# Kernel tuning notes

Hardware: AMD Instinct MI355X
Metric: run time of the kernel (lower is better)

Reference implementation:

```python
import jax, jax.numpy as jnp
import numpy as np

N = 100000      # num POIs (nodes)
M = 20000       # num trajectories (hyperedges)
NNZ = 1000000   # incidence entries
D = 128         # emb_dim
NUM_LAYERS = 3
NEG_SLOPE = 0.2  # PyG HypergraphConv leaky_relu default


def setup_inputs() -> dict:
    key = jax.random.key(0)
    ks = jax.random.split(key, 8)
    pois_embs = jax.random.normal(ks[0], (N, D), jnp.float32)
    traj_embs = jax.random.normal(ks[1], (M, D), jnp.float32)
    hyperedge_weight = jax.random.uniform(ks[2], (M,), jnp.float32)
    node_idx = jax.random.randint(ks[3], (NNZ,), 0, N, jnp.int32)
    edge_idx = jax.random.randint(ks[4], (NNZ,), 0, M, jnp.int32)
    # learned params of the shared HypergraphConv layer (heads=1, concat)
    W_lin = jax.random.normal(ks[5], (D, D), jnp.float32) / np.sqrt(D).astype(np.float32)
    att = jax.random.normal(ks[6], (2 * D,), jnp.float32) * 0.1
    bias = jnp.zeros((D,), jnp.float32)
    return dict(pois_embs=pois_embs, traj_embs=traj_embs,
                hyperedge_weight=hyperedge_weight,
                node_idx=node_idx, edge_idx=edge_idx,
                W_lin=W_lin, att=att, bias=bias)


def _segment_softmax(scores, seg, num_seg):
    smax = jax.ops.segment_max(scores, seg, num_segments=num_seg)
    smax = jnp.where(jnp.isfinite(smax), smax, 0.0)  # guard empty segments
    ex = jnp.exp(scores - smax[seg])
    den = jax.ops.segment_sum(ex, seg, num_segments=num_seg)
    return ex / (den[seg] + 1e-16)


def _hconv(x, traj_embs, hyperedge_weight, node_idx, edge_idx, W_lin, att, bias):
    # x: [N, D] node feats; traj_embs: [M, D] hyperedge feats
    xt = x @ W_lin            # [N, D]  lin(x)
    et = traj_embs @ W_lin    # [M, D]  lin(hyperedge_attr)
    # attention logits per incidence pair (additive decomposition of cat*att)
    s_n = xt @ att[:D]        # [N]
    s_e = et @ att[D:]        # [M]
    alpha = jax.nn.leaky_relu(s_n[node_idx] + s_e[edge_idx], NEG_SLOPE)  # [NNZ]
    alpha = _segment_softmax(alpha, node_idx, N)  # softmax grouped by node
    # degree normalizations: D = sum_e H_ve * w_e, B = |e|
    Ddeg = jax.ops.segment_sum(hyperedge_weight[edge_idx], node_idx, num_segments=N)
    Dinv = jnp.where(Ddeg > 0, 1.0 / Ddeg, 0.0)
    Bdeg = jax.ops.segment_sum(jnp.ones((NNZ,), xt.dtype), edge_idx, num_segments=M)
    Binv = jnp.where(Bdeg > 0, 1.0 / Bdeg, 0.0)
    # node -> edge: B^{-1} H^T (alpha * x)
    msg1 = (alpha * Binv[edge_idx])[:, None] * xt[node_idx]        # [NNZ, D]
    edge_out = jax.ops.segment_sum(msg1, edge_idx, num_segments=M)  # [M, D]
    # edge -> node: D^{-1} H (alpha * edge_out)
    msg2 = (alpha * Dinv[node_idx])[:, None] * edge_out[edge_idx]   # [NNZ, D]
    out = jax.ops.segment_sum(msg2, node_idx, num_segments=N)       # [N, D]
    return out + bias


def reference(pois_embs, traj_embs, hyperedge_weight, node_idx, edge_idx, W_lin, att, bias):
    cur = pois_embs
    acc = pois_embs  # running sum of stacked layer outputs (incl. input)
    for _ in range(NUM_LAYERS):
        cur = _hconv(cur, traj_embs, hyperedge_weight, node_idx, edge_idx, W_lin, att, bias) + cur
        acc = acc + cur
    return acc / jnp.asarray(NUM_LAYERS + 1, acc.dtype)  # mean over stack
```

## Files before the change

### kernel.cpp

```cpp
#include <hip/hip_runtime.h>
#include <hip/hip_fp16.h>
#include <cstdint>
#include <cstddef>
#include <cstring>

#define DIM 128
#define NEG_SLOPE 0.2f

#define EREP 16
#define NREP 8

typedef _Float16 half8v __attribute__((ext_vector_type(8)));
typedef __attribute__((ext_vector_type(4))) float float4v;

__device__ __forceinline__ float2 h2f2(uint u) {
  __half2 h;
  __builtin_memcpy(&h, &u, 4);
  return __half22float2(h);
}
__device__ __forceinline__ uint packh2(float lo, float hi) {
  __half2 h = __floats2half2_rn(lo, hi);
  uint u;
  __builtin_memcpy(&u, &h, 4);
  return u;
}
__device__ __forceinline__ ushort f2h_us(float f) {
  __half h = __float2half_rn(f);
  ushort us;
  __builtin_memcpy(&us, &h, 2);
  return us;
}
__device__ __forceinline__ float lrelu(float x) {
  return x >= 0.0f ? x : NEG_SLOPE * x;
}

__global__ void wswz_kernel(const float* __restrict__ W, ushort* __restrict__ Wswz)
{
  int i = blockIdx.x * 256 + threadIdx.x;
  int j = i & 7, lane = (i >> 3) & 63, nt = (i >> 9) & 7, kt = i >> 12;
  int k = kt * 32 + (lane >> 4) * 8 + j;
  int col = nt * 16 + (lane & 15);
  Wswz[i] = f2h_us(W[k * 128 + col]);
}

__global__ void poish_kernel(const float* __restrict__ pois,
                             uint4* __restrict__ pois_h, int N_, int NP)
{
  int i = blockIdx.x * 256 + threadIdx.x;
  if (i >= NP * 16) return;
  int row = i >> 4;
  uint4 o;
  if (row < N_) {
    const float* src = pois + (size_t)i * 8;
    float4 f0 = *(const float4*)src;
    float4 f1 = *(const float4*)(src + 4);
    o.x = packh2(f0.x, f0.y); o.y = packh2(f0.z, f0.w);
    o.z = packh2(f1.x, f1.y); o.w = packh2(f1.z, f1.w);
  } else { o.x = o.y = o.z = o.w = 0; }
  pois_h[i] = o;
}

__global__ __launch_bounds__(256) void gemm_mfma_kernel(
    const ushort* __restrict__ Xb, const ushort* __restrict__ Wswz,
    const float* __restrict__ att, ushort* __restrict__ Yb,
    float* __restrict__ s_n, int rowsN)
{
  __shared__ ushort st[64 * 128];
  int tid = threadIdx.x;
  int w = tid >> 6, lane = tid & 63;
  int q = lane >> 4, c = lane & 15;
  int r0b = blockIdx.x * 64;
  int r0 = r0b + w * 16;
  float4v acc[8];
#pragma unroll
  for (int nt = 0; nt < 8; ++nt) acc[nt] = (float4v){0.f, 0.f, 0.f, 0.f};
  const ushort* arow = Xb + (size_t)(r0 + c) * DIM + q * 8;
#pragma unroll
  for (int kt = 0; kt < 4; ++kt) {
    half8v a = *(const half8v*)(arow + kt * 32);
#pragma unroll
    for (int nt = 0; nt < 8; ++nt) {
      half8v b = *(const half8v*)(Wswz + ((((kt << 3) + nt) << 9) + (lane << 3)));
      acc[nt] = __builtin_amdgcn_mfma_f32_16x16x32_f16(a, b, acc[nt], 0, 0, 0);
    }
  }
  float av[8];
#pragma unroll
  for (int nt = 0; nt < 8; ++nt) av[nt] = att[nt * 16 + c];
  float p0 = 0, p1 = 0, p2 = 0, p3 = 0;
#pragma unroll
  for (int nt = 0; nt < 8; ++nt) {
    p0 = fmaf(acc[nt][0], av[nt], p0);
    p1 = fmaf(acc[nt][1], av[nt], p1);
    p2 = fmaf(acc[nt][2], av[nt], p2);
    p3 = fmaf(acc[nt][3], av[nt], p3);
  }
#pragma unroll
  for (int m = 8; m >= 1; m >>= 1) {
    p0 += __shfl_xor(p0, m, 64);
    p1 += __shfl_xor(p1, m, 64);
    p2 += __shfl_xor(p2, m, 64);
    p3 += __shfl_xor(p3, m, 64);
  }
  if (c == 0) {
    int rb = r0 + q * 4;
    if (rb + 0 < rowsN) s_n[rb + 0] = p0;
    if (rb + 1 < rowsN) s_n[rb + 1] = p1;
    if (rb + 2 < rowsN) s_n[rb + 2] = p2;
    if (rb + 3 < rowsN) s_n[rb + 3] = p3;
  }
  ushort* sw = st + w * 2048;
#pragma unroll
  for (int nt = 0; nt < 8; ++nt) {
    sw[(q * 4 + 0) * 128 + nt * 16 + c] = f2h_us(acc[nt][0]);
    sw[(q * 4 + 1) * 128 + nt * 16 + c] = f2h_us(acc[nt][1]);
    sw[(q * 4 + 2) * 128 + nt * 16 + c] = f2h_us(acc[nt][2]);
    sw[(q * 4 + 3) * 128 + nt * 16 + c] = f2h_us(acc[nt][3]);
  }
  __syncthreads();
#pragma unroll
  for (int it = 0; it < 4; ++it) {
    int idx = tid + it * 256;
    int row = idx >> 4, seg = idx & 15;
    *(uint4*)(Yb + (size_t)(r0b + row) * DIM + seg * 8) =
        *(const uint4*)&st[row * 128 + seg * 8];
  }
}

__global__ __launch_bounds__(256) void se_kernel(
    const float* __restrict__ traj, const float* __restrict__ W,
    const float* __restrict__ att, const float* __restrict__ hw,
    float* __restrict__ s_e, float2* __restrict__ se_hw, int M_)
{
  __shared__ float wv[128];
  int tid = threadIdx.x;
  if (tid < 128) {
    const float* wr = W + (size_t)tid * 128;
    float acc = 0.0f;
#pragma unroll 4
    for (int k = 0; k < 128; ++k) acc = fmaf(wr[k], att[DIM + k], acc);
    wv[tid] = acc;
  }
  __syncthreads();
  int e = blockIdx.x * 4 + (tid >> 6);
  int lane = tid & 63;
  if (e >= M_) return;
  const float* row = traj + (size_t)e * DIM;
  float v = row[lane] * wv[lane] + row[lane + 64] * wv[lane + 64];
#pragma unroll
  for (int d = 32; d > 0; d >>= 1) v += __shfl_down(v, d, 64);
  if (lane == 0) {
    s_e[e] = v;
    float2 g; g.x = v; g.y = hw[e];
    se_hw[e] = g;
  }
}

__global__ void hist_rank_kernel(const int* __restrict__ node_idx,
                                 const int* __restrict__ edge_idx,
                                 int* __restrict__ ncnt_r, int* __restrict__ ecnt_r,
                                 int* __restrict__ r_n, int* __restrict__ r_e,
                                 int nnz, int M_, int N_)
{
  int t = blockIdx.x * blockDim.x + threadIdx.x;
  int j = t * 2;
  if (j >= nnz) return;
  int* ec = ecnt_r + (size_t)(t & (EREP - 1)) * M_;
  int* nc = ncnt_r + (size_t)(t & (NREP - 1)) * N_;
  if (j + 2 <= nnz) {
    int2 e = *(const int2*)&edge_idx[j];
    int2 n = *(const int2*)&node_idx[j];
    int a0 = atomicAdd(&ec[e.x], 1);
    int a1 = atomicAdd(&ec[e.y], 1);
    int b0 = atomicAdd(&nc[n.x], 1);
    int b1 = atomicAdd(&nc[n.y], 1);
    *(int2*)&r_e[j] = make_int2(a0, a1);
    *(int2*)&r_n[j] = make_int2(b0, b1);
  } else {
    r_e[j] = atomicAdd(&ec[edge_idx[j]], 1);
    r_n[j] = atomicAdd(&nc[node_idx[j]], 1);
  }
}

__global__ void repsum_kernel(int* __restrict__ cnt_r, int* __restrict__ cnt,
                              int nbins, int reps)
{
  int b = blockIdx.x * blockDim.x + threadIdx.x;
  if (b >= nbins) return;
  int s = 0;
  for (int r = 0; r < reps; ++r) {
    size_t o = (size_t)r * nbins + b;
    int v = cnt_r[o];
    cnt_r[o] = s;
    s += v;
  }
  cnt[b] = s;
}

__global__ __launch_bounds__(1024) void scan_block_kernel(
    const int* __restrict__ cnt, int* __restrict__ off,
    int* __restrict__ partials, int nbins)
{
  __shared__ int ws[16];
  int tid = threadIdx.x, lane = tid & 63, wid = tid >> 6;
  int base = blockIdx.x * 4096 + tid * 4;
  int x0 = base + 0 < nbins ? cnt[base + 0] : 0;
  int x1 = base + 1 < nbins ? cnt[base + 1] : 0;
  int x2 = base + 2 < nbins ? cnt[base + 2] : 0;
  int x3 = base + 3 < nbins ? cnt[base + 3] : 0;
  int t = x0 + x1 + x2 + x3;
  int v = t;
#pragma unroll
  for (int d = 1; d < 64; d <<= 1) {
    int y = __shfl_up(v, d, 64);
    if (lane >= d) v += y;
  }
  if (lane == 63) ws[wid] = v;
  __syncthreads();
  if (tid < 16) {
    int s = ws[tid];
#pragma unroll
    for (int d = 1; d < 16; d <<= 1) {
      int y = __shfl_up(s, d, 16);
      if (tid >= d) s += y;
    }
    ws[tid] = s;
  }
  __syncthreads();
  int pre = (wid > 0 ? ws[wid - 1] : 0) + (v - t);
  if (base + 0 < nbins) off[base + 0] = pre;
  if (base + 1 < nbins) off[base + 1] = pre + x0;
  if (base + 2 < nbins) off[base + 2] = pre + x0 + x1;
  if (base + 3 < nbins) off[base + 3] = pre + x0 + x1 + x2;
  if (tid == 0) partials[blockIdx.x] = ws[15];
}

__global__ __launch_bounds__(64) void scan_partials_kernel(
    int* __restrict__ partials, int nb)
{
  int lane = threadIdx.x;
  int t = lane < nb ? partials[lane] : 0;
  int v = t;
#pragma unroll
  for (int d = 1; d < 64; d <<= 1) {
    int y = __shfl_up(v, d, 64);
    if (lane >= d) v += y;
  }
  if (lane < nb) partials[lane] = v - t;
  if (lane == 63) partials[nb] = v;
}

__global__ void add_off_combine_kernel(int* __restrict__ off,
                                       const int* __restrict__ partials,
                                       int* __restrict__ pre,
                                       int nbins, int nb, int reps)
{
  int i = blockIdx.x * blockDim.x + threadIdx.x;
  if (i < nbins) {
    int o = off[i] + partials[i >> 12];
    off[i] = o;
    for (int r = 0; r < reps; ++r) pre[(size_t)r * nbins + i] += o;
  }
  if (i == 0) off[nbins] = partials[nb];
}

__global__ void scatter_edge_kernel(const int* __restrict__ node_idx,
                                    const int* __restrict__ edge_idx,
                                    const int* __restrict__ r_e,
                                    const int* __restrict__ pre_e,
                                    int* __restrict__ nd_e, int nnz, int M_)
{
  int j = (blockIdx.x * blockDim.x + threadIdx.x) * 4;
  if (j >= nnz) return;
  if (j + 4 <= nnz) {
    const int* p0 = pre_e + (size_t)((j >> 1) & (EREP - 1)) * M_;
    const int* p1 = pre_e + (size_t)(((j >> 1) + 1) & (EREP - 1)) * M_;
    int4 e = *(const int4*)&edge_idx[j];
    int4 n = *(const int4*)&node_idx[j];
    int4 re = *(const int4*)&r_e[j];
    nd_e[p0[e.x] + re.x] = n.x;
    nd_e[p0[e.y] + re.y] = n.y;
    nd_e[p1[e.z] + re.z] = n.z;
    nd_e[p1[e.w] + re.w] = n.w;
  } else {
    for (int k = j; k < nnz; ++k) {
      const int* pp = pre_e + (size_t)((k >> 1) & (EREP - 1)) * M_;
      nd_e[pp[edge_idx[k]] + r_e[k]] = node_idx[k];
    }
  }
}

__global__ void scatter_node_kernel(const int* __restrict__ node_idx,
                                    const int* __restrict__ edge_idx,
                                    const int* __restrict__ r_n,
                                    const int* __restrict__ pre_n,
                                    int* __restrict__ eidx_n, int nnz, int N_)
{
  int j = (blockIdx.x * blockDim.x + threadIdx.x) * 4;
  if (j >= nnz) return;
  if (j + 4 <= nnz) {
    const int* p0 = pre_n + (size_t)((j >> 1) & (NREP - 1)) * N_;
    const int* p1 = pre_n + (size_t)(((j >> 1) + 1) & (NREP - 1)) * N_;
    int4 e = *(const int4*)&edge_idx[j];
    int4 n = *(const int4*)&node_idx[j];
    int4 rn = *(const int4*)&r_n[j];
    eidx_n[p0[n.x] + rn.x] = e.x;
    eidx_n[p0[n.y] + rn.y] = e.y;
    eidx_n[p1[n.z] + rn.z] = e.z;
    eidx_n[p1[n.w] + rn.w] = e.w;
  } else {
    for (int k = j; k < nnz; ++k) {
      const int* pp = pre_n + (size_t)((k >> 1) & (NREP - 1)) * N_;
      eidx_n[pp[node_idx[k]] + r_n[k]] = edge_idx[k];
    }
  }
}

__global__ void softstat_kernel(const int* __restrict__ noff,
                                const int* __restrict__ eidx_n,
                                const float* __restrict__ s_n,
                                const float2* __restrict__ se_hw,
                                float2* __restrict__ ns2,
                                float* __restrict__ Dinv, int N_)
{
  int n = blockIdx.x * blockDim.x + threadIdx.x;
  if (n >= N_) return;
  int s = noff[n], e1 = noff[n + 1];
  float sn = s_n[n];
  float m = -INFINITY, den = 0.0f, d = 0.0f;
  int t = s;
  for (; t + 4 <= e1; t += 4) {
    int i0 = eidx_n[t], i1 = eidx_n[t + 1], i2 = eidx_n[t + 2], i3 = eidx_n[t + 3];
    float2 g0 = se_hw[i0], g1 = se_hw[i1], g2 = se_hw[i2], g3 = se_hw[i3];
    float l0 = lrelu(sn + g0.x), l1 = lrelu(sn + g1.x);
    float l2 = lrelu(sn + g2.x), l3 = lrelu(sn + g3.x);
    float mm = fmaxf(fmaxf(fmaxf(l0, l1), fmaxf(l2, l3)), m);
    den = den * __expf(m - mm) + __expf(l0 - mm) + __expf(l1 - mm)
        + __expf(l2 - mm) + __expf(l3 - mm);
    m = mm;
    d += g0.y + g1.y + g2.y + g3.y;
  }
  for (; t < e1; ++t) {
    float2 g = se_hw[eidx_n[t]];
    float l = lrelu(sn + g.x);
    float mm = fmaxf(l, m);
    den = den * __expf(m - mm) + __expf(l - mm);
    m = mm;
    d += g.y;
  }
  if (s == e1) m = 0.0f;
  float2 r;
  r.x = sn;
  r.y = m + __logf(den + 1e-16f);
  ns2[n] = r;
  Dinv[n] = d > 0.0f ? 1.0f / d : 0.0f;
}

__global__ __launch_bounds__(256) void msg1_kernel(
    const int* __restrict__ eoff, const int* __restrict__ nd_e,
    const float2* __restrict__ ns2, const float* __restrict__ s_e,
    const uint4* __restrict__ xt16, uint4* __restrict__ eo16, int M_)
{
  int e = blockIdx.x * 4 + (threadIdx.x >> 6);
  int lane = threadIdx.x & 63;
  int r = lane >> 4, c = lane & 15;
  if (e >= M_) return;
  int s = eoff[e], t1 = eoff[e + 1];
  int len = t1 - s;
  float binv = len > 0 ? 1.0f / (float)len : 0.0f;
  float se = s_e[e];
  float acc[8];
#pragma unroll
  for (int j = 0; j < 8; ++j) acc[j] = 0.0f;
  for (int t = s; t < t1; t += 8) {
#pragma unroll
    for (int h = 0; h < 2; ++h) {
      int tb = t + h * 4;
      if (tb < t1) {
        int ti = tb + r;
        int tc = ti < t1 ? ti : t1 - 1;
        float valid = ti < t1 ? 1.0f : 0.0f;
        int nd = nd_e[tc];
        float2 q = ns2[nd];
        float coef = valid * __expf(lrelu(q.x + se) - q.y);
        uint4 g = xt16[(size_t)nd * 16 + c];
        float2 f0 = h2f2(g.x), f1 = h2f2(g.y), f2 = h2f2(g.z), f3 = h2f2(g.w);
        acc[0] = fmaf(coef, f0.x, acc[0]);
        acc[1] = fmaf(coef, f0.y, acc[1]);
        acc[2] = fmaf(coef, f1.x, acc[2]);
        acc[3] = fmaf(coef, f1.y, acc[3]);
        acc[4] = fmaf(coef, f2.x, acc[4]);
        acc[5] = fmaf(coef, f2.y, acc[5]);
        acc[6] = fmaf(coef, f3.x, acc[6]);
        acc[7] = fmaf(coef, f3.y, acc[7]);
      }
    }
  }
#pragma unroll
  for (int j = 0; j < 8; ++j) {
    acc[j] += __shfl_xor(acc[j], 16, 64);
    acc[j] += __shfl_xor(acc[j], 32, 64);
  }
  if (r == 0) {
    uint4 o;
    o.x = packh2(acc[0] * binv, acc[1] * binv);
    o.y = packh2(acc[2] * binv, acc[3] * binv);
    o.z = packh2(acc[4] * binv, acc[5] * binv);
    o.w = packh2(acc[6] * binv, acc[7] * binv);
    eo16[(size_t)e * 16 + c] = o;
  }
}

__global__ __launch_bounds__(256) void msg2_kernel(
    const int* __restrict__ noff, const int* __restrict__ eidx_n,
    const float2* __restrict__ ns2, const float* __restrict__ Dinv,
    const float* __restrict__ s_e, const uint4* __restrict__ eo16,
    const float* __restrict__ bias,
    const float* __restrict__ cin_f, const uint4* __restrict__ cin_h16,
    const uint4* __restrict__ x1h16, const uint4* __restrict__ x2h16,
    uint4* __restrict__ couth16, float* __restrict__ dout,
    int mode, int N_)
{
  int n = blockIdx.x * 4 + (threadIdx.x >> 6);
  int lane = threadIdx.x & 63;
  int r = lane >> 4, c = lane & 15;
  if (n >= N_) return;
  int s = noff[n], t1 = noff[n + 1];
  float2 nsv = ns2[n];
  float sn = nsv.x, lz = nsv.y;
  float acc[8];
#pragma unroll
  for (int j = 0; j < 8; ++j) acc[j] = 0.0f;
  for (int t = s; t < t1; t += 8) {
#pragma unroll
    for (int h = 0; h < 2; ++h) {
      int tb = t + h * 4;
      if (tb < t1) {
        int ti = tb + r;
        int tc = ti < t1 ? ti : t1 - 1;
        float valid = ti < t1 ? 1.0f : 0.0f;
        int ed = eidx_n[tc];
        float xs = s_e[ed];
        float coef = valid * __expf(lrelu(sn + xs) - lz);
        uint4 g = eo16[(size_t)ed * 16 + c];
        float2 f0 = h2f2(g.x), f1 = h2f2(g.y), f2 = h2f2(g.z), f3 = h2f2(g.w);
        acc[0] = fmaf(coef, f0.x, acc[0]);
        acc[1] = fmaf(coef, f0.y, acc[1]);
        acc[2] = fmaf(coef, f1.x, acc[2]);
        acc[3] = fmaf(coef, f1.y, acc[3]);
        acc[4] = fmaf(coef, f2.x, acc[4]);
        acc[5] = fmaf(coef, f2.y, acc[5]);
        acc[6] = fmaf(coef, f3.x, acc[6]);
        acc[7] = fmaf(coef, f3.y, acc[7]);
      }
    }
  }
#pragma unroll
  for (int j = 0; j < 8; ++j) {
    acc[j] += __shfl_xor(acc[j], 16, 64);
    acc[j] += __shfl_xor(acc[j], 32, 64);
  }
  if (r != 0) return;
  float sc = Dinv[n];
  float cin[8];
  if (mode == 0) {
    const float4* cf = (const float4*)(cin_f + (size_t)n * DIM);
    float4 a = cf[c * 2], b = cf[c * 2 + 1];
    cin[0] = a.x; cin[1] = a.y; cin[2] = a.z; cin[3] = a.w;
    cin[4] = b.x; cin[5] = b.y; cin[6] = b.z; cin[7] = b.w;
  } else {
    uint4 ch = cin_h16[(size_t)n * 16 + c];
    float2 p0 = h2f2(ch.x), p1 = h2f2(ch.y), p2 = h2f2(ch.z), p3 = h2f2(ch.w);
    cin[0] = p0.x; cin[1] = p0.y; cin[2] = p1.x; cin[3] = p1.y;
    cin[4] = p2.x; cin[5] = p2.y; cin[6] = p3.x; cin[7] = p3.y;
  }
  const float4* bf = (const float4*)bias;
  float4 ba = bf[c * 2], bb = bf[c * 2 + 1];
  float bs[8] = {ba.x, ba.y, ba.z, ba.w, bb.x, bb.y, bb.z, bb.w};
  float cx[8];
#pragma unroll
  for (int j = 0; j < 8; ++j) cx[j] = cin[j] + acc[j] * sc + bs[j];
  if (mode == 2) {
    uint4 x1 = x1h16[(size_t)n * 16 + c];
    float2 z0 = h2f2(x1.x), z1 = h2f2(x1.y), z2 = h2f2(x1.z), z3 = h2f2(x1.w);
    float x1v[8] = {z0.x, z0.y, z1.x, z1.y, z2.x, z2.y, z3.x, z3.y};
    uint4 x2 = x2h16[(size_t)n * 16 + c];
    float2 y0 = h2f2(x2.x), y1 = h2f2(x2.y), y2 = h2f2(x2.z), y3 = h2f2(x2.w);
    float x2v[8] = {y0.x, y0.y, y1.x, y1.y, y2.x, y2.y, y3.x, y3.y};
    float4 o0, o1;
    o0.x = (x1v[0] + x2v[0] + cin[0] + cx[0]) * 0.25f;
    o0.y = (x1v[1] + x2v[1] + cin[1] + cx[1]) * 0.25f;
    o0.z = (x1v[2] + x2v[2] + cin[2] + cx[2]) * 0.25f;
    o0.w = (x1v[3] + x2v[3] + cin[3] + cx[3]) * 0.25f;
    o1.x = (x1v[4] + x2v[4] + cin[4] + cx[4]) * 0.25f;
    o1.y = (x1v[5] + x2v[5] + cin[5] + cx[5]) * 0.25f;
    o1.z = (x1v[6] + x2v[6] + cin[6] + cx[6]) * 0.25f;
    o1.w = (x1v[7] + x2v[7] + cin[7] + cx[7]) * 0.25f;
    float4* dp = (float4*)(dout + (size_t)n * DIM);
    dp[c * 2] = o0;
    dp[c * 2 + 1] = o1;
  } else {
    uint4 o;
    o.x = packh2(cx[0], cx[1]);
    o.y = packh2(cx[2], cx[3]);
    o.z = packh2(cx[4], cx[5]);
    o.w = packh2(cx[6], cx[7]);
    couth16[(size_t)n * 16 + c] = o;
  }
}

static inline int cdiv(int a, int b) { return (a + b - 1) / b; }

extern "C" void kernel_launch(void* const* d_in, const int* in_sizes, int n_in,
                              void* d_out, int out_size, void* d_ws, size_t ws_size,
                              hipStream_t stream)
{
  const float* pois = (const float*)d_in[0];
  const float* traj = (const float*)d_in[1];
  const float* hw   = (const float*)d_in[2];
  const int* node_idx = (const int*)d_in[3];
  const int* edge_idx = (const int*)d_in[4];
  const float* W    = (const float*)d_in[5];
  const float* att  = (const float*)d_in[6];
  const float* bias = (const float*)d_in[7];
  float* dout = (float*)d_out;

  const int N   = in_sizes[0] / DIM;
  const int M   = in_sizes[2];
  const int NNZ = in_sizes[3];
  const int NP  = (N + 63) & ~63;

  char* p = (char*)d_ws;
  auto alloc = [&](size_t bytes) -> void* {
    void* r = (void*)p;
    p += (bytes + 255) & ~(size_t)255;
    return r;
  };
  ushort* xt_h    = (ushort*)alloc((size_t)NP * DIM * 2);
  ushort* pois_h  = (ushort*)alloc((size_t)NP * DIM * 2);
  uint*   cura_h  = (uint*)alloc((size_t)NP * 64 * 4);
  uint*   curb_h  = (uint*)alloc((size_t)NP * 64 * 4);
  ushort* W_swz   = (ushort*)alloc(16384 * 2);
  uint*   eo_h  = (uint*)alloc((size_t)M * (DIM / 2) * 4);
  float2* ns2   = (float2*)alloc((size_t)N * 8);
  float*  s_e  = (float*)alloc((size_t)M * 4);
  float2* se_hw = (float2*)alloc((size_t)M * 8);
  float*  s_n  = (float*)alloc((size_t)N * 4);
  float*  Dinv = (float*)alloc((size_t)N * 4);
  int* ecnt   = (int*)alloc((size_t)M * 4);
  int* ncnt   = (int*)alloc((size_t)N * 4);
  int* ecnt_r = (int*)alloc((size_t)EREP * M * 4);
  int* ncnt_r = (int*)alloc((size_t)NREP * N * 4);
  int* eoff = (int*)alloc((size_t)(M + 1) * 4);
  int* noff = (int*)alloc((size_t)(N + 1) * 4);
  int* r_e  = (int*)alloc((size_t)NNZ * 4);
  int* r_n  = (int*)alloc((size_t)NNZ * 4);
  int* nd_e   = (int*)alloc((size_t)NNZ * 4);
  int* eidx_n = (int*)alloc((size_t)NNZ * 4);
  int* part_e = (int*)alloc(65 * 4);
  int* part_n = (int*)alloc(65 * 4);
  (void)ws_size;

  const int nbE = cdiv(M, 4096), nbN = cdiv(N, 4096);

  hipMemsetAsync(ecnt_r, 0, (size_t)EREP * M * 4, stream);
  hipMemsetAsync(ncnt_r, 0, (size_t)NREP * N * 4, stream);
  hist_rank_kernel<<<cdiv(NNZ, 512), 256, 0, stream>>>(node_idx, edge_idx, ncnt_r, ecnt_r, r_n, r_e, NNZ, M, N);
  repsum_kernel<<<cdiv(M, 256), 256, 0, stream>>>(ecnt_r, ecnt, M, EREP);
  repsum_kernel<<<cdiv(N, 256), 256, 0, stream>>>(ncnt_r, ncnt, N, NREP);
  scan_block_kernel<<<nbE, 1024, 0, stream>>>(ecnt, eoff, part_e, M);
  scan_block_kernel<<<nbN, 1024, 0, stream>>>(ncnt, noff, part_n, N);
  scan_partials_kernel<<<1, 64, 0, stream>>>(part_e, nbE);
  scan_partials_kernel<<<1, 64, 0, stream>>>(part_n, nbN);
  add_off_combine_kernel<<<cdiv(M, 256), 256, 0, stream>>>(eoff, part_e, ecnt_r, M, nbE, EREP);
  add_off_combine_kernel<<<cdiv(N, 256), 256, 0, stream>>>(noff, part_n, ncnt_r, N, nbN, NREP);
  scatter_edge_kernel<<<cdiv(NNZ, 1024), 256, 0, stream>>>(node_idx, edge_idx, r_e, ecnt_r, nd_e, NNZ, M);
  scatter_node_kernel<<<cdiv(NNZ, 1024), 256, 0, stream>>>(node_idx, edge_idx, r_n, ncnt_r, eidx_n, NNZ, N);

  wswz_kernel<<<64, 256, 0, stream>>>(W, W_swz);
  se_kernel<<<cdiv(M, 4), 256, 0, stream>>>(traj, W, att, hw, s_e, se_hw, M);
  poish_kernel<<<cdiv(NP * 16, 256), 256, 0, stream>>>(pois, (uint4*)pois_h, N, NP);

  for (int layer = 0; layer < 3; ++layer) {
    const ushort* gin = (layer == 0) ? pois_h
                       : (layer == 1) ? (const ushort*)cura_h
                                      : (const ushort*)curb_h;
    gemm_mfma_kernel<<<NP / 64, 256, 0, stream>>>(gin, W_swz, att, xt_h, s_n, N);
    softstat_kernel<<<cdiv(N, 256), 256, 0, stream>>>(noff, eidx_n, s_n, se_hw, ns2, Dinv, N);
    msg1_kernel<<<cdiv(M, 4), 256, 0, stream>>>(eoff, nd_e, ns2, s_e,
                                                (const uint4*)xt_h, (uint4*)eo_h, M);
    const uint* cin_h = (layer == 1) ? cura_h : curb_h;
    uint* couth = (layer == 0) ? cura_h : curb_h;
    msg2_kernel<<<cdiv(N, 4), 256, 0, stream>>>(noff, eidx_n, ns2, Dinv, s_e,
                                                (const uint4*)eo_h, bias,
                                                pois, (const uint4*)cin_h,
                                                (const uint4*)pois_h,
                                                (const uint4*)cura_h,
                                                (uint4*)couth, dout, layer, N);
  }
}
```

Measured before the change: 689.5 us.

## Fuse histogram, first-layer GEMM and edge-score kernels into one launch

```diff
diff --git a/kernel.cpp b/kernel.cpp
--- a/kernel.cpp
+++ b/kernel.cpp
@@ -60,6 +60,135 @@
   pois_h[i] = o;
 }
 
+__global__ __launch_bounds__(256) void prep_fused_kernel(
+    const int* __restrict__ node_idx, const int* __restrict__ edge_idx,
+    int* __restrict__ ncnt_r, int* __restrict__ ecnt_r,
+    int* __restrict__ r_n, int* __restrict__ r_e,
+    int nnz, int M_, int N_, int histBlocks,
+    const ushort* __restrict__ Xb, const ushort* __restrict__ Wswz,
+    const float* __restrict__ att, ushort* __restrict__ Yb,
+    float* __restrict__ s_n, int rowsN, int gemmBlocks,
+    const float* __restrict__ traj, const float* __restrict__ W,
+    const float* __restrict__ hw,
+    float* __restrict__ s_e, float2* __restrict__ se_hw)
+{
+  __shared__ ushort st[64 * 128];
+  int b = blockIdx.x;
+  int tid = threadIdx.x;
+
+  if (b < histBlocks) {
+    int T = b * 256 + tid;
+    int stride = histBlocks * 256;
+    int npairs = (nnz + 1) >> 1;
+    for (int t = T; t < npairs; t += stride) {
+      int j = t * 2;
+      int* ec = ecnt_r + (size_t)(t & (EREP - 1)) * M_;
+      int* nc = ncnt_r + (size_t)(t & (NREP - 1)) * N_;
+      if (j + 2 <= nnz) {
+        int2 e = *(const int2*)&edge_idx[j];
+        int2 n = *(const int2*)&node_idx[j];
+        int a0 = atomicAdd(&ec[e.x], 1);
+        int a1 = atomicAdd(&ec[e.y], 1);
+        int b0 = atomicAdd(&nc[n.x], 1);
+        int b1 = atomicAdd(&nc[n.y], 1);
+        *(int2*)&r_e[j] = make_int2(a0, a1);
+        *(int2*)&r_n[j] = make_int2(b0, b1);
+      } else {
+        r_e[j] = atomicAdd(&ec[edge_idx[j]], 1);
+        r_n[j] = atomicAdd(&nc[node_idx[j]], 1);
+      }
+    }
+    return;
+  }
+
+  if (b < histBlocks + gemmBlocks) {
+    int bb = b - histBlocks;
+    int w = tid >> 6, lane = tid & 63;
+    int q = lane >> 4, c = lane & 15;
+    int r0b = bb * 64;
+    int r0 = r0b + w * 16;
+    float4v acc[8];
+#pragma unroll
+    for (int nt = 0; nt < 8; ++nt) acc[nt] = (float4v){0.f, 0.f, 0.f, 0.f};
+    const ushort* arow = Xb + (size_t)(r0 + c) * DIM + q * 8;
+#pragma unroll
+    for (int kt = 0; kt < 4; ++kt) {
+      half8v a = *(const half8v*)(arow + kt * 32);
+#pragma unroll
+      for (int nt = 0; nt < 8; ++nt) {
+        half8v bfr = *(const half8v*)(Wswz + ((((kt << 3) + nt) << 9) + (lane << 3)));
+        acc[nt] = __builtin_amdgcn_mfma_f32_16x16x32_f16(a, bfr, acc[nt], 0, 0, 0);
+      }
+    }
+    float av[8];
+#pragma unroll
+    for (int nt = 0; nt < 8; ++nt) av[nt] = att[nt * 16 + c];
+    float p0 = 0, p1 = 0, p2 = 0, p3 = 0;
+#pragma unroll
+    for (int nt = 0; nt < 8; ++nt) {
+      p0 = fmaf(acc[nt][0], av[nt], p0);
+      p1 = fmaf(acc[nt][1], av[nt], p1);
+      p2 = fmaf(acc[nt][2], av[nt], p2);
+      p3 = fmaf(acc[nt][3], av[nt], p3);
+    }
+#pragma unroll
+    for (int m = 8; m >= 1; m >>= 1) {
+      p0 += __shfl_xor(p0, m, 64);
+      p1 += __shfl_xor(p1, m, 64);
+      p2 += __shfl_xor(p2, m, 64);
+      p3 += __shfl_xor(p3, m, 64);
+    }
+    if (c == 0) {
+      int rb = r0 + q * 4;
+      if (rb + 0 < rowsN) s_n[rb + 0] = p0;
+      if (rb + 1 < rowsN) s_n[rb + 1] = p1;
+      if (rb + 2 < rowsN) s_n[rb + 2] = p2;
+      if (rb + 3 < rowsN) s_n[rb + 3] = p3;
+    }
+    ushort* sw = st + w * 2048;
+#pragma unroll
+    for (int nt = 0; nt < 8; ++nt) {
+      sw[(q * 4 + 0) * 128 + nt * 16 + c] = f2h_us(acc[nt][0]);
+      sw[(q * 4 + 1) * 128 + nt * 16 + c] = f2h_us(acc[nt][1]);
+      sw[(q * 4 + 2) * 128 + nt * 16 + c] = f2h_us(acc[nt][2]);
+      sw[(q * 4 + 3) * 128 + nt * 16 + c] = f2h_us(acc[nt][3]);
+    }
+    __syncthreads();
+#pragma unroll
+    for (int it = 0; it < 4; ++it) {
+      int idx = tid + it * 256;
+      int row = idx >> 4, seg = idx & 15;
+      *(uint4*)(Yb + (size_t)(r0b + row) * DIM + seg * 8) =
+          *(const uint4*)&st[row * 128 + seg * 8];
+    }
+    return;
+  }
+
+  {
+    float* wv = (float*)st;
+    if (tid < 128) {
+      const float* wr = W + (size_t)tid * 128;
+      float acc = 0.0f;
+#pragma unroll 4
+      for (int k = 0; k < 128; ++k) acc = fmaf(wr[k], att[DIM + k], acc);
+      wv[tid] = acc;
+    }
+    __syncthreads();
+    int e = (b - histBlocks - gemmBlocks) * 4 + (tid >> 6);
+    int lane = tid & 63;
+    if (e >= M_) return;
+    const float* row = traj + (size_t)e * DIM;
+    float v = row[lane] * wv[lane] + row[lane + 64] * wv[lane + 64];
+#pragma unroll
+    for (int d = 32; d > 0; d >>= 1) v += __shfl_down(v, d, 64);
+    if (lane == 0) {
+      s_e[e] = v;
+      float2 g; g.x = v; g.y = hw[e];
+      se_hw[e] = g;
+    }
+  }
+}
+
 __global__ __launch_bounds__(256) void gemm_mfma_kernel(
     const ushort* __restrict__ Xb, const ushort* __restrict__ Wswz,
     const float* __restrict__ att, ushort* __restrict__ Yb,
@@ -124,61 +253,6 @@
     int row = idx >> 4, seg = idx & 15;
     *(uint4*)(Yb + (size_t)(r0b + row) * DIM + seg * 8) =
         *(const uint4*)&st[row * 128 + seg * 8];
-  }
-}
-
-__global__ __launch_bounds__(256) void se_kernel(
-    const float* __restrict__ traj, const float* __restrict__ W,
-    const float* __restrict__ att, const float* __restrict__ hw,
-    float* __restrict__ s_e, float2* __restrict__ se_hw, int M_)
-{
-  __shared__ float wv[128];
-  int tid = threadIdx.x;
-  if (tid < 128) {
-    const float* wr = W + (size_t)tid * 128;
-    float acc = 0.0f;
-#pragma unroll 4
-    for (int k = 0; k < 128; ++k) acc = fmaf(wr[k], att[DIM + k], acc);
-    wv[tid] = acc;
-  }
-  __syncthreads();
-  int e = blockIdx.x * 4 + (tid >> 6);
-  int lane = tid & 63;
-  if (e >= M_) return;
-  const float* row = traj + (size_t)e * DIM;
-  float v = row[lane] * wv[lane] + row[lane + 64] * wv[lane + 64];
-#pragma unroll
-  for (int d = 32; d > 0; d >>= 1) v += __shfl_down(v, d, 64);
-  if (lane == 0) {
-    s_e[e] = v;
-    float2 g; g.x = v; g.y = hw[e];
-    se_hw[e] = g;
-  }
-}
-
-__global__ void hist_rank_kernel(const int* __restrict__ node_idx,
-                                 const int* __restrict__ edge_idx,
-                                 int* __restrict__ ncnt_r, int* __restrict__ ecnt_r,
-                                 int* __restrict__ r_n, int* __restrict__ r_e,
-                                 int nnz, int M_, int N_)
-{
-  int t = blockIdx.x * blockDim.x + threadIdx.x;
-  int j = t * 2;
-  if (j >= nnz) return;
-  int* ec = ecnt_r + (size_t)(t & (EREP - 1)) * M_;
-  int* nc = ncnt_r + (size_t)(t & (NREP - 1)) * N_;
-  if (j + 2 <= nnz) {
-    int2 e = *(const int2*)&edge_idx[j];
-    int2 n = *(const int2*)&node_idx[j];
-    int a0 = atomicAdd(&ec[e.x], 1);
-    int a1 = atomicAdd(&ec[e.y], 1);
-    int b0 = atomicAdd(&nc[n.x], 1);
-    int b1 = atomicAdd(&nc[n.y], 1);
-    *(int2*)&r_e[j] = make_int2(a0, a1);
-    *(int2*)&r_n[j] = make_int2(b0, b1);
-  } else {
-    r_e[j] = atomicAdd(&ec[edge_idx[j]], 1);
-    r_n[j] = atomicAdd(&nc[node_idx[j]], 1);
   }
 }
 
@@ -416,7 +490,7 @@
     const float2* __restrict__ ns2, const float* __restrict__ Dinv,
     const float* __restrict__ s_e, const uint4* __restrict__ eo16,
     const float* __restrict__ bias,
-    const float* __restrict__ cin_f, const uint4* __restrict__ cin_h16,
+    const uint4* __restrict__ cin_h16,
     const uint4* __restrict__ x1h16, const uint4* __restrict__ x2h16,
     uint4* __restrict__ couth16, float* __restrict__ dout,
     int mode, int N_)
@@ -462,18 +536,9 @@
   }
   if (r != 0) return;
   float sc = Dinv[n];
-  float cin[8];
-  if (mode == 0) {
-    const float4* cf = (const float4*)(cin_f + (size_t)n * DIM);
-    float4 a = cf[c * 2], b = cf[c * 2 + 1];
-    cin[0] = a.x; cin[1] = a.y; cin[2] = a.z; cin[3] = a.w;
-    cin[4] = b.x; cin[5] = b.y; cin[6] = b.z; cin[7] = b.w;
-  } else {
-    uint4 ch = cin_h16[(size_t)n * 16 + c];
-    float2 p0 = h2f2(ch.x), p1 = h2f2(ch.y), p2 = h2f2(ch.z), p3 = h2f2(ch.w);
-    cin[0] = p0.x; cin[1] = p0.y; cin[2] = p1.x; cin[3] = p1.y;
-    cin[4] = p2.x; cin[5] = p2.y; cin[6] = p3.x; cin[7] = p3.y;
-  }
+  uint4 ch = cin_h16[(size_t)n * 16 + c];
+  float2 p0 = h2f2(ch.x), p1 = h2f2(ch.y), p2 = h2f2(ch.z), p3 = h2f2(ch.w);
+  float cin[8] = {p0.x, p0.y, p1.x, p1.y, p2.x, p2.y, p3.x, p3.y};
   const float4* bf = (const float4*)bias;
   float4 ba = bf[c * 2], bb = bf[c * 2 + 1];
   float bs[8] = {ba.x, ba.y, ba.z, ba.w, bb.x, bb.y, bb.z, bb.w};
@@ -562,10 +627,21 @@
   (void)ws_size;
 
   const int nbE = cdiv(M, 4096), nbN = cdiv(N, 4096);
+  const int npairs = (NNZ + 1) >> 1;
+  const int histBlocks = cdiv(npairs, 512);
+  const int gemmBlocks = NP / 64;
+  const int seBlocks = cdiv(M, 4);
 
   hipMemsetAsync(ecnt_r, 0, (size_t)EREP * M * 4, stream);
   hipMemsetAsync(ncnt_r, 0, (size_t)NREP * N * 4, stream);
-  hist_rank_kernel<<<cdiv(NNZ, 512), 256, 0, stream>>>(node_idx, edge_idx, ncnt_r, ecnt_r, r_n, r_e, NNZ, M, N);
+  wswz_kernel<<<64, 256, 0, stream>>>(W, W_swz);
+  poish_kernel<<<cdiv(NP * 16, 256), 256, 0, stream>>>(pois, (uint4*)pois_h, N, NP);
+
+  prep_fused_kernel<<<histBlocks + gemmBlocks + seBlocks, 256, 0, stream>>>(
+      node_idx, edge_idx, ncnt_r, ecnt_r, r_n, r_e, NNZ, M, N, histBlocks,
+      pois_h, W_swz, att, xt_h, s_n, N, gemmBlocks,
+      traj, W, hw, s_e, se_hw);
+
   repsum_kernel<<<cdiv(M, 256), 256, 0, stream>>>(ecnt_r, ecnt, M, EREP);
   repsum_kernel<<<cdiv(N, 256), 256, 0, stream>>>(ncnt_r, ncnt, N, NREP);
   scan_block_kernel<<<nbE, 1024, 0, stream>>>(ecnt, eoff, part_e, M);
@@ -577,23 +653,21 @@
   scatter_edge_kernel<<<cdiv(NNZ, 1024), 256, 0, stream>>>(node_idx, edge_idx, r_e, ecnt_r, nd_e, NNZ, M);
   scatter_node_kernel<<<cdiv(NNZ, 1024), 256, 0, stream>>>(node_idx, edge_idx, r_n, ncnt_r, eidx_n, NNZ, N);
 
-  wswz_kernel<<<64, 256, 0, stream>>>(W, W_swz);
-  se_kernel<<<cdiv(M, 4), 256, 0, stream>>>(traj, W, att, hw, s_e, se_hw, M);
-  poish_kernel<<<cdiv(NP * 16, 256), 256, 0, stream>>>(pois, (uint4*)pois_h, N, NP);
-
   for (int layer = 0; layer < 3; ++layer) {
-    const ushort* gin = (layer == 0) ? pois_h
-                       : (layer == 1) ? (const ushort*)cura_h
-                                      : (const ushort*)curb_h;
-    gemm_mfma_kernel<<<NP / 64, 256, 0, stream>>>(gin, W_swz, att, xt_h, s_n, N);
+    if (layer > 0) {
+      const ushort* gin = (layer == 1) ? (const ushort*)cura_h
+                                       : (const ushort*)curb_h;
+      gemm_mfma_kernel<<<NP / 64, 256, 0, stream>>>(gin, W_swz, att, xt_h, s_n, N);
+    }
     softstat_kernel<<<cdiv(N, 256), 256, 0, stream>>>(noff, eidx_n, s_n, se_hw, ns2, Dinv, N);
     msg1_kernel<<<cdiv(M, 4), 256, 0, stream>>>(eoff, nd_e, ns2, s_e,
                                                 (const uint4*)xt_h, (uint4*)eo_h, M);
-    const uint* cin_h = (layer == 1) ? cura_h : curb_h;
+    const uint* cin_h = (layer == 0) ? (const uint*)pois_h
+                       : (layer == 1) ? cura_h : curb_h;
     uint* couth = (layer == 0) ? cura_h : curb_h;
     msg2_kernel<<<cdiv(N, 4), 256, 0, stream>>>(noff, eidx_n, ns2, Dinv, s_e,
                                                 (const uint4*)eo_h, bias,
-                                                pois, (const uint4*)cin_h,
+                                                (const uint4*)cin_h,
                                                 (const uint4*)pois_h,
                                                 (const uint4*)cura_h,
                                                 (uint4*)couth, dout, layer, N);
```

Measured after the change: 679.7 us. Within noise of the previous version (-1.4%).

## Drop replicated histograms and fuse histogram with edge-score kernel

Applied to the files above, without the earlier changes.

```diff
diff --git a/kernel.cpp b/kernel.cpp
--- a/kernel.cpp
+++ b/kernel.cpp
@@ -6,9 +6,6 @@
 
 #define DIM 128
 #define NEG_SLOPE 0.2f
-
-#define EREP 16
-#define NREP 8
 
 typedef _Float16 half8v __attribute__((ext_vector_type(8)));
 typedef __attribute__((ext_vector_type(4))) float float4v;
@@ -60,6 +57,61 @@
   pois_h[i] = o;
 }
 
+__global__ __launch_bounds__(256) void hist_se_fused_kernel(
+    const int* __restrict__ node_idx, const int* __restrict__ edge_idx,
+    int* __restrict__ ncnt, int* __restrict__ ecnt,
+    int* __restrict__ r_n, int* __restrict__ r_e,
+    int nnz, int M_, int N_, int histBlocks,
+    const float* __restrict__ traj, const float* __restrict__ W,
+    const float* __restrict__ att, const float* __restrict__ hw,
+    float* __restrict__ s_e, float2* __restrict__ se_hw)
+{
+  __shared__ float wv[128];
+  int b = blockIdx.x;
+  int tid = threadIdx.x;
+
+  if (b < histBlocks) {
+    int t = b * 256 + tid;
+    int j = t * 2;
+    if (j >= nnz) return;
+    if (j + 2 <= nnz) {
+      int2 e = *(const int2*)&edge_idx[j];
+      int2 n = *(const int2*)&node_idx[j];
+      int a0 = atomicAdd(&ecnt[e.x], 1);
+      int a1 = atomicAdd(&ecnt[e.y], 1);
+      int b0 = atomicAdd(&ncnt[n.x], 1);
+      int b1 = atomicAdd(&ncnt[n.y], 1);
+      *(int2*)&r_e[j] = make_int2(a0, a1);
+      *(int2*)&r_n[j] = make_int2(b0, b1);
+    } else {
+      r_e[j] = atomicAdd(&ecnt[edge_idx[j]], 1);
+      r_n[j] = atomicAdd(&ncnt[node_idx[j]], 1);
+    }
+    return;
+  }
+
+  if (tid < 128) {
+    const float* wr = W + (size_t)tid * 128;
+    float acc = 0.0f;
+#pragma unroll 4
+    for (int k = 0; k < 128; ++k) acc = fmaf(wr[k], att[DIM + k], acc);
+    wv[tid] = acc;
+  }
+  __syncthreads();
+  int e = (b - histBlocks) * 4 + (tid >> 6);
+  int lane = tid & 63;
+  if (e >= M_) return;
+  const float* row = traj + (size_t)e * DIM;
+  float v = row[lane] * wv[lane] + row[lane + 64] * wv[lane + 64];
+#pragma unroll
+  for (int d = 32; d > 0; d >>= 1) v += __shfl_down(v, d, 64);
+  if (lane == 0) {
+    s_e[e] = v;
+    float2 g; g.x = v; g.y = hw[e];
+    se_hw[e] = g;
+  }
+}
+
 __global__ __launch_bounds__(256) void gemm_mfma_kernel(
     const ushort* __restrict__ Xb, const ushort* __restrict__ Wswz,
     const float* __restrict__ att, ushort* __restrict__ Yb,
@@ -125,76 +177,6 @@
     *(uint4*)(Yb + (size_t)(r0b + row) * DIM + seg * 8) =
         *(const uint4*)&st[row * 128 + seg * 8];
   }
-}
-
-__global__ __launch_bounds__(256) void se_kernel(
-    const float* __restrict__ traj, const float* __restrict__ W,
-    const float* __restrict__ att, const float* __restrict__ hw,
-    float* __restrict__ s_e, float2* __restrict__ se_hw, int M_)
-{
-  __shared__ float wv[128];
-  int tid = threadIdx.x;
-  if (tid < 128) {
-    const float* wr = W + (size_t)tid * 128;
-    float acc = 0.0f;
-#pragma unroll 4
-    for (int k = 0; k < 128; ++k) acc = fmaf(wr[k], att[DIM + k], acc);
-    wv[tid] = acc;
-  }
-  __syncthreads();
-  int e = blockIdx.x * 4 + (tid >> 6);
-  int lane = tid & 63;
-  if (e >= M_) return;
-  const float* row = traj + (size_t)e * DIM;
-  float v = row[lane] * wv[lane] + row[lane + 64] * wv[lane + 64];
-#pragma unroll
-  for (int d = 32; d > 0; d >>= 1) v += __shfl_down(v, d, 64);
-  if (lane == 0) {
-    s_e[e] = v;
-    float2 g; g.x = v; g.y = hw[e];
-    se_hw[e] = g;
-  }
-}
-
-__global__ void hist_rank_kernel(const int* __restrict__ node_idx,
-                                 const int* __restrict__ edge_idx,
-                                 int* __restrict__ ncnt_r, int* __restrict__ ecnt_r,
-                                 int* __restrict__ r_n, int* __restrict__ r_e,
-                                 int nnz, int M_, int N_)
-{
-  int t = blockIdx.x * blockDim.x + threadIdx.x;
-  int j = t * 2;
-  if (j >= nnz) return;
-  int* ec = ecnt_r + (size_t)(t & (EREP - 1)) * M_;
-  int* nc = ncnt_r + (size_t)(t & (NREP - 1)) * N_;
-  if (j + 2 <= nnz) {
-    int2 e = *(const int2*)&edge_idx[j];
-    int2 n = *(const int2*)&node_idx[j];
-    int a0 = atomicAdd(&ec[e.x], 1);
-    int a1 = atomicAdd(&ec[e.y], 1);
-    int b0 = atomicAdd(&nc[n.x], 1);
-    int b1 = atomicAdd(&nc[n.y], 1);
-    *(int2*)&r_e[j] = make_int2(a0, a1);
-    *(int2*)&r_n[j] = make_int2(b0, b1);
-  } else {
-    r_e[j] = atomicAdd(&ec[edge_idx[j]], 1);
-    r_n[j] = atomicAdd(&nc[node_idx[j]], 1);
-  }
-}
-
-__global__ void repsum_kernel(int* __restrict__ cnt_r, int* __restrict__ cnt,
-                              int nbins, int reps)
-{
-  int b = blockIdx.x * blockDim.x + threadIdx.x;
-  if (b >= nbins) return;
-  int s = 0;
-  for (int r = 0; r < reps; ++r) {
-    size_t o = (size_t)r * nbins + b;
-    int v = cnt_r[o];
-    cnt_r[o] = s;
-    s += v;
-  }
-  cnt[b] = s;
 }
 
 __global__ __launch_bounds__(1024) void scan_block_kernel(
@@ -250,69 +232,54 @@
   if (lane == 63) partials[nb] = v;
 }
 
-__global__ void add_off_combine_kernel(int* __restrict__ off,
-                                       const int* __restrict__ partials,
-                                       int* __restrict__ pre,
-                                       int nbins, int nb, int reps)
+__global__ void add_off_kernel(int* __restrict__ off,
+                               const int* __restrict__ partials,
+                               int nbins, int nb)
 {
   int i = blockIdx.x * blockDim.x + threadIdx.x;
-  if (i < nbins) {
-    int o = off[i] + partials[i >> 12];
-    off[i] = o;
-    for (int r = 0; r < reps; ++r) pre[(size_t)r * nbins + i] += o;
-  }
+  if (i < nbins) off[i] += partials[i >> 12];
   if (i == 0) off[nbins] = partials[nb];
 }
 
 __global__ void scatter_edge_kernel(const int* __restrict__ node_idx,
                                     const int* __restrict__ edge_idx,
                                     const int* __restrict__ r_e,
-                                    const int* __restrict__ pre_e,
-                                    int* __restrict__ nd_e, int nnz, int M_)
+                                    const int* __restrict__ eoff,
+                                    int* __restrict__ nd_e, int nnz)
 {
   int j = (blockIdx.x * blockDim.x + threadIdx.x) * 4;
   if (j >= nnz) return;
   if (j + 4 <= nnz) {
-    const int* p0 = pre_e + (size_t)((j >> 1) & (EREP - 1)) * M_;
-    const int* p1 = pre_e + (size_t)(((j >> 1) + 1) & (EREP - 1)) * M_;
     int4 e = *(const int4*)&edge_idx[j];
     int4 n = *(const int4*)&node_idx[j];
     int4 re = *(const int4*)&r_e[j];
-    nd_e[p0[e.x] + re.x] = n.x;
-    nd_e[p0[e.y] + re.y] = n.y;
-    nd_e[p1[e.z] + re.z] = n.z;
-    nd_e[p1[e.w] + re.w] = n.w;
+    nd_e[eoff[e.x] + re.x] = n.x;
+    nd_e[eoff[e.y] + re.y] = n.y;
+    nd_e[eoff[e.z] + re.z] = n.z;
+    nd_e[eoff[e.w] + re.w] = n.w;
   } else {
-    for (int k = j; k < nnz; ++k) {
-      const int* pp = pre_e + (size_t)((k >> 1) & (EREP - 1)) * M_;
-      nd_e[pp[edge_idx[k]] + r_e[k]] = node_idx[k];
-    }
+    for (int k = j; k < nnz; ++k) nd_e[eoff[edge_idx[k]] + r_e[k]] = node_idx[k];
   }
 }
 
 __global__ void scatter_node_kernel(const int* __restrict__ node_idx,
                                     const int* __restrict__ edge_idx,
                                     const int* __restrict__ r_n,
-                                    const int* __restrict__ pre_n,
-                                    int* __restrict__ eidx_n, int nnz, int N_)
+                                    const int* __restrict__ noff,
+                                    int* __restrict__ eidx_n, int nnz)
 {
   int j = (blockIdx.x * blockDim.x + threadIdx.x) * 4;
   if (j >= nnz) return;
   if (j + 4 <= nnz) {
-    const int* p0 = pre_n + (size_t)((j >> 1) & (NREP - 1)) * N_;
-    const int* p1 = pre_n + (size_t)(((j >> 1) + 1) & (NREP - 1)) * N_;
     int4 e = *(const int4*)&edge_idx[j];
     int4 n = *(const int4*)&node_idx[j];
     int4 rn = *(const int4*)&r_n[j];
-    eidx_n[p0[n.x] + rn.x] = e.x;
-    eidx_n[p0[n.y] + rn.y] = e.y;
-    eidx_n[p1[n.z] + rn.z] = e.z;
-    eidx_n[p1[n.w] + rn.w] = e.w;
+    eidx_n[noff[n.x] + rn.x] = e.x;
+    eidx_n[noff[n.y] + rn.y] = e.y;
+    eidx_n[noff[n.z] + rn.z] = e.z;
+    eidx_n[noff[n.w] + rn.w] = e.w;
   } else {
-    for (int k = j; k < nnz; ++k) {
-      const int* pp = pre_n + (size_t)((k >> 1) & (NREP - 1)) * N_;
-      eidx_n[pp[node_idx[k]] + r_n[k]] = edge_idx[k];
-    }
+    for (int k = j; k < nnz; ++k) eidx_n[noff[node_idx[k]] + r_n[k]] = edge_idx[k];
   }
 }
 
@@ -416,7 +383,7 @@
     const float2* __restrict__ ns2, const float* __restrict__ Dinv,
     const float* __restrict__ s_e, const uint4* __restrict__ eo16,
     const float* __restrict__ bias,
-    const float* __restrict__ cin_f, const uint4* __restrict__ cin_h16,
+    const uint4* __restrict__ cin_h16,
     const uint4* __restrict__ x1h16, const uint4* __restrict__ x2h16,
     uint4* __restrict__ couth16, float* __restrict__ dout,
     int mode, int N_)
@@ -462,18 +429,9 @@
   }
   if (r != 0) return;
   float sc = Dinv[n];
-  float cin[8];
-  if (mode == 0) {
-    const float4* cf = (const float4*)(cin_f + (size_t)n * DIM);
-    float4 a = cf[c * 2], b = cf[c * 2 + 1];
-    cin[0] = a.x; cin[1] = a.y; cin[2] = a.z; cin[3] = a.w;
-    cin[4] = b.x; cin[5] = b.y; cin[6] = b.z; cin[7] = b.w;
-  } else {
-    uint4 ch = cin_h16[(size_t)n * 16 + c];
-    float2 p0 = h2f2(ch.x), p1 = h2f2(ch.y), p2 = h2f2(ch.z), p3 = h2f2(ch.w);
-    cin[0] = p0.x; cin[1] = p0.y; cin[2] = p1.x; cin[3] = p1.y;
-    cin[4] = p2.x; cin[5] = p2.y; cin[6] = p3.x; cin[7] = p3.y;
-  }
+  uint4 ch = cin_h16[(size_t)n * 16 + c];
+  float2 p0 = h2f2(ch.x), p1 = h2f2(ch.y), p2 = h2f2(ch.z), p3 = h2f2(ch.w);
+  float cin[8] = {p0.x, p0.y, p1.x, p1.y, p2.x, p2.y, p3.x, p3.y};
   const float4* bf = (const float4*)bias;
   float4 ba = bf[c * 2], bb = bf[c * 2 + 1];
   float bs[8] = {ba.x, ba.y, ba.z, ba.w, bb.x, bb.y, bb.z, bb.w};
@@ -547,10 +505,8 @@
   float2* se_hw = (float2*)alloc((size_t)M * 8);
   float*  s_n  = (float*)alloc((size_t)N * 4);
   float*  Dinv = (float*)alloc((size_t)N * 4);
-  int* ecnt   = (int*)alloc((size_t)M * 4);
-  int* ncnt   = (int*)alloc((size_t)N * 4);
-  int* ecnt_r = (int*)alloc((size_t)EREP * M * 4);
-  int* ncnt_r = (int*)alloc((size_t)NREP * N * 4);
+  int* ecnt = (int*)alloc((size_t)M * 4);
+  int* ncnt = (int*)alloc((size_t)N * 4);
   int* eoff = (int*)alloc((size_t)(M + 1) * 4);
   int* noff = (int*)alloc((size_t)(N + 1) * 4);
   int* r_e  = (int*)alloc((size_t)NNZ * 4);
@@ -562,24 +518,26 @@
   (void)ws_size;
 
   const int nbE = cdiv(M, 4096), nbN = cdiv(N, 4096);
-
-  hipMemsetAsync(ecnt_r, 0, (size_t)EREP * M * 4, stream);
-  hipMemsetAsync(ncnt_r, 0, (size_t)NREP * N * 4, stream);
-  hist_rank_kernel<<<cdiv(NNZ, 512), 256, 0, stream>>>(node_idx, edge_idx, ncnt_r, ecnt_r, r_n, r_e, NNZ, M, N);
-  repsum_kernel<<<cdiv(M, 256), 256, 0, stream>>>(ecnt_r, ecnt, M, EREP);
-  repsum_kernel<<<cdiv(N, 256), 256, 0, stream>>>(ncnt_r, ncnt, N, NREP);
+  const int histBlocks = cdiv(NNZ, 512);
+  const int seBlocks = cdiv(M, 4);
+
+  hipMemsetAsync(ecnt, 0, (size_t)M * 4, stream);
+  hipMemsetAsync(ncnt, 0, (size_t)N * 4, stream);
+  wswz_kernel<<<64, 256, 0, stream>>>(W, W_swz);
+  poish_kernel<<<cdiv(NP * 16, 256), 256, 0, stream>>>(pois, (uint4*)pois_h, N, NP);
+
+  hist_se_fused_kernel<<<histBlocks + seBlocks, 256, 0, stream>>>(
+      node_idx, edge_idx, ncnt, ecnt, r_n, r_e, NNZ, M, N, histBlocks,
+      traj, W, att, hw, s_e, se_hw);
+
   scan_block_kernel<<<nbE, 1024, 0, stream>>>(ecnt, eoff, part_e, M);
   scan_block_kernel<<<nbN, 1024, 0, stream>>>(ncnt, noff, part_n, N);
   scan_partials_kernel<<<1, 64, 0, stream>>>(part_e, nbE);
   scan_partials_kernel<<<1, 64, 0, stream>>>(part_n, nbN);
-  add_off_combine_kernel<<<cdiv(M, 256), 256, 0, stream>>>(eoff, part_e, ecnt_r, M, nbE, EREP);
-  add_off_combine_kernel<<<cdiv(N, 256), 256, 0, stream>>>(noff, part_n, ncnt_r, N, nbN, NREP);
-  scatter_edge_kernel<<<cdiv(NNZ, 1024), 256, 0, stream>>>(node_idx, edge_idx, r_e, ecnt_r, nd_e, NNZ, M);
-  scatter_node_kernel<<<cdiv(NNZ, 1024), 256, 0, stream>>>(node_idx, edge_idx, r_n, ncnt_r, eidx_n, NNZ, N);
-
-  wswz_kernel<<<64, 256, 0, stream>>>(W, W_swz);
-  se_kernel<<<cdiv(M, 4), 256, 0, stream>>>(traj, W, att, hw, s_e, se_hw, M);
-  poish_kernel<<<cdiv(NP * 16, 256), 256, 0, stream>>>(pois, (uint4*)pois_h, N, NP);
+  add_off_kernel<<<cdiv(M, 256), 256, 0, stream>>>(eoff, part_e, M, nbE);
+  add_off_kernel<<<cdiv(N, 256), 256, 0, stream>>>(noff, part_n, N, nbN);
+  scatter_edge_kernel<<<cdiv(NNZ, 1024), 256, 0, stream>>>(node_idx, edge_idx, r_e, eoff, nd_e, NNZ);
+  scatter_node_kernel<<<cdiv(NNZ, 1024), 256, 0, stream>>>(node_idx, edge_idx, r_n, noff, eidx_n, NNZ);
 
   for (int layer = 0; layer < 3; ++layer) {
     const ushort* gin = (layer == 0) ? pois_h
@@ -589,11 +547,12 @@
     softstat_kernel<<<cdiv(N, 256), 256, 0, stream>>>(noff, eidx_n, s_n, se_hw, ns2, Dinv, N);
     msg1_kernel<<<cdiv(M, 4), 256, 0, stream>>>(eoff, nd_e, ns2, s_e,
                                                 (const uint4*)xt_h, (uint4*)eo_h, M);
-    const uint* cin_h = (layer == 1) ? cura_h : curb_h;
+    const uint* cin_h = (layer == 0) ? (const uint*)pois_h
+                       : (layer == 1) ? cura_h : curb_h;
     uint* couth = (layer == 0) ? cura_h : curb_h;
     msg2_kernel<<<cdiv(N, 4), 256, 0, stream>>>(noff, eidx_n, ns2, Dinv, s_e,
                                                 (const uint4*)eo_h, bias,
-                                                pois, (const uint4*)cin_h,
+                                                (const uint4*)cin_h,
                                                 (const uint4*)pois_h,
                                                 (const uint4*)cura_h,
                                                 (uint4*)couth, dout, layer, N);
```

Result: faster. 665.1 us (-3.5%).
